# Optimization experiments

Measured on AMD Instinct MI355X. Metric: run time of the kernel, lower is better.

Reference implementation:

```python
import jax, jax.numpy as jnp
import numpy as np

N = 100000
D = 64
FE = 8
E = 1600000


def setup_inputs() -> dict:
    key = jax.random.key(0)
    ks = jax.random.split(key, 24)
    s = 0.05
    inp = {
        "H_adapted_t": jax.random.normal(ks[0], (N, D), jnp.float32),
        "event_vector": jax.random.normal(ks[1], (N, FE), jnp.float32),
        "edge_index": jax.random.randint(ks[2], (2, E), 0, N, jnp.int32),
        # event encoder MLP
        "enc_W1": jax.random.normal(ks[3], (FE, D), jnp.float32) * s,
        "enc_b1": jnp.zeros((D,), jnp.float32),
        "enc_W2": jax.random.normal(ks[4], (D, D), jnp.float32) * s,
        "enc_b2": jnp.zeros((D,), jnp.float32),
        # GCNConv
        "gcn_W": jax.random.normal(ks[5], (D, D), jnp.float32) * s,
        "gcn_b": jnp.zeros((D,), jnp.float32),
        # GATConv (heads=1, concat=False)
        "gat_W": jax.random.normal(ks[6], (D, D), jnp.float32) * s,
        "gat_att_src": jax.random.normal(ks[7], (D,), jnp.float32) * s,
        "gat_att_dst": jax.random.normal(ks[8], (D,), jnp.float32) * s,
        "gat_b": jnp.zeros((D,), jnp.float32),
        # gate fusion
        "gate_W": jax.random.normal(ks[9], (2 * D, D), jnp.float32) * s,
        "gate_b": jnp.zeros((D,), jnp.float32),
        # residual decoder
        "res_W1": jax.random.normal(ks[10], (2 * D, D), jnp.float32) * s,
        "res_b1": jnp.zeros((D,), jnp.float32),
        "res_W2": jax.random.normal(ks[11], (D, D), jnp.float32) * s,
        "res_b2": jnp.zeros((D,), jnp.float32),
        # speed head
        "sp_W1": jax.random.normal(ks[12], (D, 32), jnp.float32) * s,
        "sp_b1": jnp.zeros((32,), jnp.float32),
        "sp_W2": jax.random.normal(ks[13], (32, 1), jnp.float32) * s,
        "sp_b2": jnp.zeros((1,), jnp.float32),
    }
    return inp


def _gcn(x, src, dst, W, b, n):
    # PyG GCNConv: x' = D^{-1/2} (A + I) D^{-1/2} X W + b
    h = x @ W
    deg = jax.ops.segment_sum(jnp.ones_like(dst, jnp.float32), dst, num_segments=n)
    dinv = jnp.where(deg > 0, jax.lax.rsqrt(jnp.maximum(deg, 1e-12)), 0.0)
    norm = dinv[src] * dinv[dst]  # [E+N]
    out = jax.ops.segment_sum(h[src] * norm[:, None], dst, num_segments=n)
    return out + b


def _gat(x, src, dst, W, att_src, att_dst, b, n):
    # PyG GATConv (1 head): alpha = softmax_dst(leaky_relu(a_s.Wx_src + a_d.Wx_dst))
    h = x @ W
    a_s = h @ att_src  # [n]
    a_d = h @ att_dst
    e = jax.nn.leaky_relu(a_s[src] + a_d[dst], negative_slope=0.2)  # [E+N]
    m = jax.ops.segment_max(e, dst, num_segments=n)
    ex = jnp.exp(e - m[dst])
    z = jax.ops.segment_sum(ex, dst, num_segments=n)
    alpha = ex / z[dst]
    out = jax.ops.segment_sum(h[src] * alpha[:, None], dst, num_segments=n)
    return out + b


def reference(H_adapted_t, event_vector, edge_index,
              enc_W1, enc_b1, enc_W2, enc_b2,
              gcn_W, gcn_b,
              gat_W, gat_att_src, gat_att_dst, gat_b,
              gate_W, gate_b,
              res_W1, res_b1, res_W2, res_b2,
              sp_W1, sp_b1, sp_W2, sp_b2):
    n = H_adapted_t.shape[0]
    # add self-loops (PyG default for both convs)
    loop = jnp.arange(n, dtype=edge_index.dtype)
    src = jnp.concatenate([edge_index[0], loop])
    dst = jnp.concatenate([edge_index[1], loop])

    # event encoder
    emb = jax.nn.relu(event_vector @ enc_W1 + enc_b1) @ enc_W2 + enc_b2
    # diffusion: GCN -> ReLU -> GAT -> ReLU
    x = jax.nn.relu(_gcn(emb, src, dst, gcn_W, gcn_b, n))
    diffused = jax.nn.relu(_gat(x, src, dst, gat_W, gat_att_src, gat_att_dst, gat_b, n))

    fusion = jnp.concatenate([H_adapted_t, diffused], axis=-1)  # [N, 2D]
    gate = jax.nn.sigmoid(fusion @ gate_W + gate_b)
    delta_raw = jax.nn.relu(fusion @ res_W1 + res_b1) @ res_W2 + res_b2
    delta = gate * delta_raw
    H_final = H_adapted_t + delta
    pred_speed = (jax.nn.relu(H_final @ sp_W1 + sp_b1) @ sp_W2 + sp_b2)[:, 0]
    return (delta, H_final, pred_speed)
```

## Files before the change

### kernel.cpp

```cpp
#include <hip/hip_runtime.h>
#include <hip/hip_bf16.h>

#define NN 100000
#define DD 64
#define FEE 8
#define EE 1600000

#define NBUCK 391
#define BCAP 6144
#define CHA 4096
#define NBLKA ((EE + CHA - 1) / CHA)

typedef __attribute__((ext_vector_type(8))) short bf16x8;
typedef __attribute__((ext_vector_type(4))) float f32x4;
typedef __attribute__((ext_vector_type(2))) float f32x2;

__device__ __forceinline__ float b2f(unsigned short u) {
    return __uint_as_float(((unsigned)u) << 16);
}
__device__ __forceinline__ unsigned short f2b(float f) {
    unsigned u = __float_as_uint(f);
    unsigned r = 0x7fffu + ((u >> 16) & 1u);
    return (unsigned short)((u + r) >> 16);
}
__device__ __forceinline__ float lrelu(float v) { return v > 0.f ? v : 0.2f * v; }
__device__ __forceinline__ unsigned fkey(float x) {
    unsigned b = __float_as_uint(x);
    return (b & 0x80000000u) ? ~b : (b | 0x80000000u);
}
__device__ __forceinline__ float funkey(unsigned u) {
    unsigned b = (u & 0x80000000u) ? (u & 0x7fffffffu) : ~u;
    return __uint_as_float(b);
}
__device__ __forceinline__ bf16x8 pack8(const float* p) {
    const float4 a = *(const float4*)p;
    const float4 b = *(const float4*)(p + 4);
    bf16x8 r;
    r[0] = (short)f2b(a.x); r[1] = (short)f2b(a.y);
    r[2] = (short)f2b(a.z); r[3] = (short)f2b(a.w);
    r[4] = (short)f2b(b.x); r[5] = (short)f2b(b.y);
    r[6] = (short)f2b(b.z); r[7] = (short)f2b(b.w);
    return r;
}

__device__ __forceinline__ float deq8(unsigned v) {
#if __has_builtin(__builtin_amdgcn_cvt_f32_fp8)
    return __builtin_amdgcn_cvt_f32_fp8(v & 0xffu, 0);
#else
    unsigned t = v & 0x7fu;
    float m = __uint_as_float(0x3C000000u + (t << 20));
    if (t < 8) m = 2.f * m - 0.015625f;
    return (v & 0x80u) ? -m : m;
#endif
}
__device__ __forceinline__ float4 deq8x4(unsigned v) {
#if __has_builtin(__builtin_amdgcn_cvt_pk_f32_fp8)
    f32x2 lo = __builtin_amdgcn_cvt_pk_f32_fp8((int)v, false);
    f32x2 hi = __builtin_amdgcn_cvt_pk_f32_fp8((int)v, true);
    return make_float4(lo[0], lo[1], hi[0], hi[1]);
#else
    return make_float4(deq8(v), deq8(v >> 8), deq8(v >> 16), deq8(v >> 24));
#endif
}
__device__ __forceinline__ unsigned q8(float f) {
    unsigned u = __float_as_uint(f);
    unsigned s = (u >> 24) & 0x80u;
    float a = fminf(__uint_as_float(u & 0x7fffffffu), 448.f);
    unsigned t;
    if (a < 0.015625f) {
        t = (unsigned)__float2int_rn(a * 512.f);
    } else {
        unsigned b = __float_as_uint(a);
        b += ((b >> 20) & 1u) + 0x7FFFFu;
        unsigned e = (b >> 23) - 120u;
        t = (e > 15u) ? 0x7Eu : (((b >> 20) & 7u) | (e << 3));
    }
    return s | t;
}
__device__ __forceinline__ unsigned pk4(float a, float b, float c, float d) {
    return q8(a) | (q8(b) << 8) | (q8(c) << 16) | (q8(d) << 24);
}

#define LK 136
#define LK2 72

__global__ __launch_bounds__(256, 4) void k_encoder_mfma(
    const float* __restrict__ ev, const float* __restrict__ W1, const float* __restrict__ b1,
    const float* __restrict__ W2, const float* __restrict__ b2,
    const float* __restrict__ gcnW, const float* __restrict__ dinv,
    unsigned char* __restrict__ hA8)
{
    __shared__ short sW1T[64 * 32];
    __shared__ short sW2T[64 * LK2];
    __shared__ short sGWT[64 * LK2];
    __shared__ float sb1[64], sb2[64];
    __shared__ short sStage[4][16 * LK2];

    for (int t = threadIdx.x; t < 64 * 32; t += 256) {
        int n = t >> 5, k = t & 31;
        sW1T[n * 32 + k] = (k < FEE) ? (short)f2b(W1[k * 64 + n]) : (short)0;
    }
    for (int t = threadIdx.x; t < 64 * 64; t += 256) {
        int k = t >> 6, n = t & 63;
        sW2T[n * LK2 + k] = (short)f2b(W2[t]);
        sGWT[n * LK2 + k] = (short)f2b(gcnW[t]);
    }
    if (threadIdx.x < 64) {
        sb1[threadIdx.x] = b1[threadIdx.x];
        sb2[threadIdx.x] = b2[threadIdx.x];
    }
    __syncthreads();

    const int wave = threadIdx.x >> 6;
    const int lane = threadIdx.x & 63;
    const int m16  = lane & 15;
    const int quad = lane >> 4;
    short* myStage = &sStage[wave][0];

    const int ngroups = NN / 16;
    for (int g = blockIdx.x * 4 + wave; g < ngroups; g += gridDim.x * 4) {
        const int row0 = g * 16;
        bf16x8 a0;
        #pragma unroll
        for (int i = 0; i < 8; i++) a0[i] = 0;
        if (quad == 0) a0 = pack8(ev + (size_t)(row0 + m16) * FEE);
        f32x4 acc[4];
        #pragma unroll
        for (int c = 0; c < 4; c++) {
            f32x4 z = {0.f, 0.f, 0.f, 0.f};
            acc[c] = __builtin_amdgcn_mfma_f32_16x16x32_bf16(
                a0, *(const bf16x8*)&sW1T[(c * 16 + m16) * 32 + quad * 8], z, 0, 0, 0);
        }
        #pragma unroll
        for (int c = 0; c < 4; c++) {
            int n = c * 16 + m16;
            float bb = sb1[n];
            #pragma unroll
            for (int r = 0; r < 4; r++)
                myStage[(quad * 4 + r) * LK2 + n] = (short)f2b(fmaxf(acc[c][r] + bb, 0.f));
        }
        bf16x8 af0 = *(const bf16x8*)&myStage[m16 * LK2 + quad * 8];
        bf16x8 af1 = *(const bf16x8*)&myStage[m16 * LK2 + 32 + quad * 8];
        #pragma unroll
        for (int c = 0; c < 4; c++) {
            f32x4 z = {0.f, 0.f, 0.f, 0.f};
            const short* bp = &sW2T[(c * 16 + m16) * LK2 + quad * 8];
            z = __builtin_amdgcn_mfma_f32_16x16x32_bf16(af0, *(const bf16x8*)bp, z, 0, 0, 0);
            acc[c] = __builtin_amdgcn_mfma_f32_16x16x32_bf16(af1, *(const bf16x8*)(bp + 32), z, 0, 0, 0);
        }
        #pragma unroll
        for (int c = 0; c < 4; c++) {
            int n = c * 16 + m16;
            float bb = sb2[n];
            #pragma unroll
            for (int r = 0; r < 4; r++)
                myStage[(quad * 4 + r) * LK2 + n] = (short)f2b(acc[c][r] + bb);
        }
        af0 = *(const bf16x8*)&myStage[m16 * LK2 + quad * 8];
        af1 = *(const bf16x8*)&myStage[m16 * LK2 + 32 + quad * 8];
        #pragma unroll
        for (int c = 0; c < 4; c++) {
            f32x4 z = {0.f, 0.f, 0.f, 0.f};
            const short* bp = &sGWT[(c * 16 + m16) * LK2 + quad * 8];
            z = __builtin_amdgcn_mfma_f32_16x16x32_bf16(af0, *(const bf16x8*)bp, z, 0, 0, 0);
            acc[c] = __builtin_amdgcn_mfma_f32_16x16x32_bf16(af1, *(const bf16x8*)(bp + 32), z, 0, 0, 0);
        }
        #pragma unroll
        for (int c = 0; c < 4; c++) {
            int n = c * 16 + m16;
            #pragma unroll
            for (int r = 0; r < 4; r++)
                myStage[(quad * 4 + r) * LK2 + n] = (short)f2b(acc[c][r]);
        }
        #pragma unroll
        for (int h = 0; h < 2; h++) {
            int row = h * 8 + (lane >> 3);
            int col = (lane & 7) * 8;
            float sc = 32.f * dinv[row0 + row];
            const short* sp = &myStage[row * LK2 + col];
            uint2 w;
            w.x = pk4(b2f(sp[0]) * sc, b2f(sp[1]) * sc, b2f(sp[2]) * sc, b2f(sp[3]) * sc);
            w.y = pk4(b2f(sp[4]) * sc, b2f(sp[5]) * sc, b2f(sp[6]) * sc, b2f(sp[7]) * sc);
            *(uint2*)(hA8 + (size_t)(row0 + row) * 64 + col) = w;
        }
    }
}

__global__ __launch_bounds__(256, 4) void k_gatw_mfma(
    const unsigned short* __restrict__ x, const float* __restrict__ gatW,
    const float* __restrict__ attS, const float* __restrict__ attD,
    unsigned char* __restrict__ hC8, float* __restrict__ a_s, float* __restrict__ a_d)
{
    __shared__ short sGWT[64 * LK2];
    __shared__ float sAS[64], sAD[64];
    __shared__ short sStage[4][16 * LK2];
    for (int t = threadIdx.x; t < 64 * 64; t += 256) {
        int k = t >> 6, n = t & 63;
        sGWT[n * LK2 + k] = (short)f2b(gatW[t]);
    }
    if (threadIdx.x < 64) {
        sAS[threadIdx.x] = attS[threadIdx.x];
        sAD[threadIdx.x] = attD[threadIdx.x];
    }
    __syncthreads();

    const int wave = threadIdx.x >> 6;
    const int lane = threadIdx.x & 63;
    const int m16  = lane & 15;
    const int quad = lane >> 4;
    short* myStage = &sStage[wave][0];

    const int ngroups = NN / 16;
    for (int g = blockIdx.x * 4 + wave; g < ngroups; g += gridDim.x * 4) {
        const int row0 = g * 16;
        const unsigned short* xr = x + (size_t)(row0 + m16) * 64 + quad * 8;
        bf16x8 af0 = *(const bf16x8*)xr;
        bf16x8 af1 = *(const bf16x8*)(xr + 32);
        f32x4 acc[4];
        #pragma unroll
        for (int c = 0; c < 4; c++) {
            f32x4 z = {0.f, 0.f, 0.f, 0.f};
            const short* bp = &sGWT[(c * 16 + m16) * LK2 + quad * 8];
            z = __builtin_amdgcn_mfma_f32_16x16x32_bf16(af0, *(const bf16x8*)bp, z, 0, 0, 0);
            acc[c] = __builtin_amdgcn_mfma_f32_16x16x32_bf16(af1, *(const bf16x8*)(bp + 32), z, 0, 0, 0);
        }
        float ps[4] = {0.f, 0.f, 0.f, 0.f}, pd[4] = {0.f, 0.f, 0.f, 0.f};
        #pragma unroll
        for (int c = 0; c < 4; c++) {
            int n = c * 16 + m16;
            float was = sAS[n], wad = sAD[n];
            #pragma unroll
            for (int r = 0; r < 4; r++) {
                float v = acc[c][r];
                myStage[(quad * 4 + r) * LK2 + n] = (short)f2b(v);
                ps[r] += v * was;
                pd[r] += v * wad;
            }
        }
        #pragma unroll
        for (int off = 1; off < 16; off <<= 1) {
            #pragma unroll
            for (int r = 0; r < 4; r++) {
                ps[r] += __shfl_xor(ps[r], off, 64);
                pd[r] += __shfl_xor(pd[r], off, 64);
            }
        }
        if (m16 == 0) {
            #pragma unroll
            for (int r = 0; r < 4; r++) {
                a_s[row0 + quad * 4 + r] = ps[r];
                a_d[row0 + quad * 4 + r] = pd[r];
            }
        }
        #pragma unroll
        for (int h = 0; h < 2; h++) {
            int row = h * 8 + (lane >> 3);
            int col = (lane & 7) * 8;
            const short* sp = &myStage[row * LK2 + col];
            uint2 w;
            w.x = pk4(b2f(sp[0]) * 32.f, b2f(sp[1]) * 32.f, b2f(sp[2]) * 32.f, b2f(sp[3]) * 32.f);
            w.y = pk4(b2f(sp[4]) * 32.f, b2f(sp[5]) * 32.f, b2f(sp[6]) * 32.f, b2f(sp[7]) * 32.f);
            *(uint2*)(hC8 + (size_t)(row0 + row) * 64 + col) = w;
        }
    }
}

__global__ __launch_bounds__(512, 4) void k_decoder_mfma(
    const float* __restrict__ H, const float* diff,
    const float* __restrict__ gateW, const float* __restrict__ gateB,
    const float* __restrict__ resW1, const float* __restrict__ resB1,
    const float* __restrict__ resW2, const float* __restrict__ resB2,
    const float* __restrict__ spW1, const float* __restrict__ spB1,
    const float* __restrict__ spW2, const float* __restrict__ spB2,
    float* outDelta, float* __restrict__ outH, float* __restrict__ outP)
{
    __shared__ short sGW[64 * LK];
    __shared__ short sRW1[64 * LK];
    __shared__ short sRW2[64 * LK2];
    __shared__ short sSW1[32 * LK2];
    __shared__ float sGB[64], sRB1[64], sRB2[64];
    __shared__ float sSB1[32], sSW2[32];
    __shared__ float sSB2;
    __shared__ short sStage[8][16 * LK2];

    for (int t = threadIdx.x; t < 128 * 64; t += 512) {
        int k = t >> 6, n = t & 63;
        sGW[n * LK + k]  = (short)f2b(gateW[t]);
        sRW1[n * LK + k] = (short)f2b(resW1[t]);
    }
    for (int t = threadIdx.x; t < 64 * 64; t += 512) {
        int k = t >> 6, n = t & 63;
        sRW2[n * LK2 + k] = (short)f2b(resW2[t]);
    }
    for (int t = threadIdx.x; t < 64 * 32; t += 512) {
        int k = t >> 5, n = t & 31;
        sSW1[n * LK2 + k] = (short)f2b(spW1[t]);
    }
    if (threadIdx.x < 64) {
        sGB[threadIdx.x]  = gateB[threadIdx.x];
        sRB1[threadIdx.x] = resB1[threadIdx.x];
        sRB2[threadIdx.x] = resB2[threadIdx.x];
    }
    if (threadIdx.x < 32) {
        sSB1[threadIdx.x] = spB1[threadIdx.x];
        sSW2[threadIdx.x] = spW2[threadIdx.x];
    }
    if (threadIdx.x == 0) sSB2 = spB2[0];
    __syncthreads();

    const int wave = threadIdx.x >> 6;
    const int lane = threadIdx.x & 63;
    const int m16  = lane & 15;
    const int quad = lane >> 4;
    short* myStage = &sStage[wave][0];

    const int ngroups = NN / 16;
    for (int g = blockIdx.x * 8 + wave; g < ngroups; g += gridDim.x * 8) {
        const int row0 = g * 16;
        const float* Hrow = H    + (size_t)(row0 + m16) * 64 + quad * 8;
        const float* Drow = diff + (size_t)(row0 + m16) * 64 + quad * 8;
        bf16x8 afrag[4];
        afrag[0] = pack8(Hrow);
        afrag[1] = pack8(Hrow + 32);
        afrag[2] = pack8(Drow);
        afrag[3] = pack8(Drow + 32);

        f32x4 accG[4], accR[4];
        #pragma unroll
        for (int c = 0; c < 4; c++) {
            f32x4 z = {0.f, 0.f, 0.f, 0.f};
            accG[c] = z; accR[c] = z;
        }
        #pragma unroll
        for (int c = 0; c < 4; c++) {
            const short* bg = &sGW[(c * 16 + m16) * LK + quad * 8];
            const short* br = &sRW1[(c * 16 + m16) * LK + quad * 8];
            #pragma unroll
            for (int t = 0; t < 4; t++) {
                bf16x8 bgf = *(const bf16x8*)(bg + 32 * t);
                accG[c] = __builtin_amdgcn_mfma_f32_16x16x32_bf16(afrag[t], bgf, accG[c], 0, 0, 0);
                bf16x8 brf = *(const bf16x8*)(br + 32 * t);
                accR[c] = __builtin_amdgcn_mfma_f32_16x16x32_bf16(afrag[t], brf, accR[c], 0, 0, 0);
            }
        }

        float gateV[4][4];
        #pragma unroll
        for (int c = 0; c < 4; c++) {
            int n = c * 16 + m16;
            float gb = sGB[n], rb = sRB1[n];
            #pragma unroll
            for (int r = 0; r < 4; r++) {
                gateV[c][r] = 1.f / (1.f + __expf(-(accG[c][r] + gb)));
                int mrow = quad * 4 + r;
                myStage[mrow * LK2 + n] = (short)f2b(fmaxf(accR[c][r] + rb, 0.f));
            }
        }
        bf16x8 h1f0 = *(const bf16x8*)&myStage[m16 * LK2 + quad * 8];
        bf16x8 h1f1 = *(const bf16x8*)&myStage[m16 * LK2 + 32 + quad * 8];

        f32x4 accD[4];
        #pragma unroll
        for (int c = 0; c < 4; c++) { f32x4 z = {0.f, 0.f, 0.f, 0.f}; accD[c] = z; }
        #pragma unroll
        for (int c = 0; c < 4; c++) {
            const short* bp = &sRW2[(c * 16 + m16) * LK2 + quad * 8];
            accD[c] = __builtin_amdgcn_mfma_f32_16x16x32_bf16(h1f0, *(const bf16x8*)bp, accD[c], 0, 0, 0);
            accD[c] = __builtin_amdgcn_mfma_f32_16x16x32_bf16(h1f1, *(const bf16x8*)(bp + 32), accD[c], 0, 0, 0);
        }

        #pragma unroll
        for (int c = 0; c < 4; c++) {
            int n = c * 16 + m16;
            float rb2 = sRB2[n];
            #pragma unroll
            for (int r = 0; r < 4; r++) {
                int mrow = quad * 4 + r;
                float delta = gateV[c][r] * (accD[c][r] + rb2);
                float hv = H[(size_t)(row0 + mrow) * 64 + n];
                float hf = hv + delta;
                outDelta[(size_t)(row0 + mrow) * 64 + n] = delta;
                outH[(size_t)(row0 + mrow) * 64 + n] = hf;
                myStage[mrow * LK2 + n] = (short)f2b(hf);
            }
        }
        bf16x8 hff0 = *(const bf16x8*)&myStage[m16 * LK2 + quad * 8];
        bf16x8 hff1 = *(const bf16x8*)&myStage[m16 * LK2 + 32 + quad * 8];

        f32x4 accS[2];
        { f32x4 z = {0.f, 0.f, 0.f, 0.f}; accS[0] = z; accS[1] = z; }
        #pragma unroll
        for (int c = 0; c < 2; c++) {
            const short* bp = &sSW1[(c * 16 + m16) * LK2 + quad * 8];
            accS[c] = __builtin_amdgcn_mfma_f32_16x16x32_bf16(hff0, *(const bf16x8*)bp, accS[c], 0, 0, 0);
            accS[c] = __builtin_amdgcn_mfma_f32_16x16x32_bf16(hff1, *(const bf16x8*)(bp + 32), accS[c], 0, 0, 0);
        }
        float part[4];
        #pragma unroll
        for (int r = 0; r < 4; r++) {
            float p0 = fmaxf(accS[0][r] + sSB1[m16], 0.f) * sSW2[m16];
            float p1 = fmaxf(accS[1][r] + sSB1[16 + m16], 0.f) * sSW2[16 + m16];
            part[r] = p0 + p1;
        }
        #pragma unroll
        for (int off = 1; off < 16; off <<= 1) {
            #pragma unroll
            for (int r = 0; r < 4; r++) part[r] += __shfl_xor(part[r], off, 64);
        }
        if (m16 == 0) {
            #pragma unroll
            for (int r = 0; r < 4; r++) outP[row0 + quad * 4 + r] = part[r] + sSB2;
        }
    }
}


__global__ __launch_bounds__(256, 2) void k_binA(
    const int* __restrict__ src, const int* __restrict__ dst,
    int* __restrict__ bcnt, int* __restrict__ bpacked)
{
    __shared__ int sCount[512];
    __shared__ int sOff[512];
    __shared__ int sCur[512];
    __shared__ int sGbase[512];
    __shared__ int sScan[256];
    __shared__ int sStage[CHA];
    __shared__ unsigned short sBkt[CHA];
    const int t = threadIdx.x;
    const int e0 = blockIdx.x * CHA;
    const int len = min(CHA, EE - e0);

    for (int i = t; i < 512; i += 256) sCount[i] = 0;
    __syncthreads();
    for (int i = t; i < len; i += 256) atomicAdd(&sCount[dst[e0 + i] >> 8], 1);
    __syncthreads();
    int a0 = sCount[2 * t], a1 = sCount[2 * t + 1];
    int pairsum = a0 + a1;
    sScan[t] = pairsum;
    __syncthreads();
    for (int off = 1; off < 256; off <<= 1) {
        int v = (t >= off) ? sScan[t - off] : 0;
        __syncthreads();
        sScan[t] += v;
        __syncthreads();
    }
    int excl = sScan[t] - pairsum;
    sOff[2 * t] = excl;       sOff[2 * t + 1] = excl + a0;
    sCur[2 * t] = excl;       sCur[2 * t + 1] = excl + a0;
    __syncthreads();
    for (int b = t; b < NBUCK; b += 256) {
        int c = sCount[b];
        sGbase[b] = c ? atomicAdd(&bcnt[b], c) : 0;
    }
    __syncthreads();
    for (int i = t; i < len; i += 256) {
        int d = dst[e0 + i];
        int s = src[e0 + i];
        int b = d >> 8;
        int p = atomicAdd(&sCur[b], 1);
        sStage[p] = ((d & 255) << 17) | s;
        sBkt[p] = (unsigned short)b;
    }
    __syncthreads();
    for (int i = t; i < len; i += 256) {
        int b = sBkt[i];
        int gp = sGbase[b] + (i - sOff[b]);
        if (gp < BCAP) bpacked[(size_t)b * BCAP + gp] = sStage[i];
    }
}

__global__ __launch_bounds__(256) void k_fillB2(
    const int* __restrict__ bcnt, const int* __restrict__ bpacked,
    int* __restrict__ row_ptr, int* __restrict__ rend, float* __restrict__ dinv,
    int* __restrict__ csr)
{
    __shared__ int lcnt[256];
    __shared__ int lscan[256];
    __shared__ int lcur[256];
    __shared__ int lstage[BCAP];
    __shared__ int sWs[4];
    __shared__ int sBase;
    const int b = blockIdx.x;
    const int t = threadIdx.x;
    const int node0 = b << 8;
    const int cnt = min(bcnt[b], BCAP);
    lcnt[t] = 0;
    int partial = 0;
    for (int i = t; i < b; i += 256) partial += bcnt[i];
    #pragma unroll
    for (int o = 32; o >= 1; o >>= 1) partial += __shfl_xor(partial, o, 64);
    if ((t & 63) == 0) sWs[t >> 6] = partial;
    __syncthreads();
    if (t == 0) sBase = sWs[0] + sWs[1] + sWs[2] + sWs[3];
    const int* bp = bpacked + (size_t)b * BCAP;
    for (int i = t; i < cnt; i += 256) atomicAdd(&lcnt[bp[i] >> 17], 1);
    __syncthreads();
    const int base = sBase;
    int own = lcnt[t];
    lscan[t] = own;
    __syncthreads();
    for (int off = 1; off < 256; off <<= 1) {
        int v = (t >= off) ? lscan[t - off] : 0;
        __syncthreads();
        lscan[t] += v;
        __syncthreads();
    }
    int excl = lscan[t] - own;
    int node = node0 + t;
    if (node < NN) {
        row_ptr[node] = base + excl;
        rend[node] = base + excl + own;
        dinv[node] = rsqrtf((float)own + 1.0f);
    }
    lcur[t] = excl;
    __syncthreads();
    for (int i = t; i < cnt; i += 256) {
        int v = bp[i];
        int p = atomicAdd(&lcur[v >> 17], 1);
        lstage[p] = v & 0x1FFFF;
    }
    __syncthreads();
    for (int i = t; i < cnt; i += 256) csr[base + i] = lstage[i];
}


__global__ __launch_bounds__(256) void k_gcn_gather(
    const int* __restrict__ row_ptr, const int* __restrict__ rend,
    const int* __restrict__ csr, const float* __restrict__ dinv,
    const unsigned char* __restrict__ hA8, const float* __restrict__ gcnB,
    unsigned short* __restrict__ x)
{
    __shared__ int2 sE[4][2][32];
    const int wave = threadIdx.x >> 6;
    const int lane = threadIdx.x & 63;
    const int half = lane >> 5;
    const int hl   = lane & 31;
    const int g2   = hl >> 4;
    const int c4   = (lane & 15) * 4;
    int2* myE = sE[wave][half];
    const float4 gb = *(const float4*)(gcnB + c4);
    const int stride = gridDim.x * 8;
    for (int node = blockIdx.x * 8 + wave * 2 + half; node < NN; node += stride) {
        const int base = row_ptr[node], end = rend[node];
        float r0 = 0.f, r1 = 0.f, r2 = 0.f, r3 = 0.f;
        for (int cb = base; cb < end; cb += 32) {
            int rem = end - cb; if (rem > 32) rem = 32;
            int sidx = 0; float w = 0.f;
            if (hl < rem) { sidx = csr[cb + hl]; w = 1.f; }
            myE[hl] = make_int2(sidx, __float_as_int(w));
            int k = 0;
            for (; k + 16 <= rem; k += 16) {
                unsigned vv[8]; float ww[8];
                #pragma unroll
                for (int j = 0; j < 8; j++) {
                    int2 e = myE[k + 2 * j + g2];
                    ww[j] = __int_as_float(e.y);
                    vv[j] = *(const unsigned*)(hA8 + (((unsigned)e.x << 6) | (unsigned)c4));
                }
                #pragma unroll
                for (int j = 0; j < 8; j++) {
                    float4 d = deq8x4(vv[j]);
                    r0 = fmaf(d.x, ww[j], r0); r1 = fmaf(d.y, ww[j], r1);
                    r2 = fmaf(d.z, ww[j], r2); r3 = fmaf(d.w, ww[j], r3);
                }
            }
            for (; k < rem; k += 8) {
                unsigned vv[4]; float ww[4];
                #pragma unroll
                for (int j = 0; j < 4; j++) {
                    int2 e = myE[k + 2 * j + g2];
                    ww[j] = __int_as_float(e.y);
                    vv[j] = *(const unsigned*)(hA8 + (((unsigned)e.x << 6) | (unsigned)c4));
                }
                #pragma unroll
                for (int j = 0; j < 4; j++) {
                    float4 d = deq8x4(vv[j]);
                    r0 = fmaf(d.x, ww[j], r0); r1 = fmaf(d.y, ww[j], r1);
                    r2 = fmaf(d.z, ww[j], r2); r3 = fmaf(d.w, ww[j], r3);
                }
            }
        }
        r0 += __shfl_xor(r0, 16, 64); r1 += __shfl_xor(r1, 16, 64);
        r2 += __shfl_xor(r2, 16, 64); r3 += __shfl_xor(r3, 16, 64);
        unsigned sv = *(const unsigned*)(hA8 + (((unsigned)node << 6) | (unsigned)c4));
        float4 sd = deq8x4(sv);
        float sc = dinv[node] * 0.03125f;
        if (g2 == 0) {
            float o0 = fmaxf(fmaf(r0 + sd.x, sc, gb.x), 0.f);
            float o1 = fmaxf(fmaf(r1 + sd.y, sc, gb.y), 0.f);
            float o2 = fmaxf(fmaf(r2 + sd.z, sc, gb.z), 0.f);
            float o3 = fmaxf(fmaf(r3 + sd.w, sc, gb.w), 0.f);
            uint2 wv;
            wv.x = (unsigned)f2b(o0) | ((unsigned)f2b(o1) << 16);
            wv.y = (unsigned)f2b(o2) | ((unsigned)f2b(o3) << 16);
            *(uint2*)(x + (size_t)node * 64 + c4) = wv;
        }
    }
}

__global__ __launch_bounds__(256) void k_gat_fused(
    const int* __restrict__ row_ptr, const int* __restrict__ rend,
    const int* __restrict__ csr,
    const float* __restrict__ a_s, const float* __restrict__ a_d,
    const unsigned char* __restrict__ hC8, const float* __restrict__ gatB,
    float* __restrict__ diff)
{
    __shared__ int2 sE[4][2][32];
    const int wave = threadIdx.x >> 6;
    const int lane = threadIdx.x & 63;
    const int half = lane >> 5;
    const int hl   = lane & 31;
    const int g2   = hl >> 4;
    const int c4   = (lane & 15) * 4;
    int2* myE = sE[wave][half];
    const float4 gb = *(const float4*)(gatB + c4);
    const int stride = gridDim.x * 8;
    for (int node = blockIdx.x * 8 + wave * 2 + half; node < NN; node += stride) {
        const int base = row_ptr[node], end = rend[node];
        const float adn = a_d[node];
        const float p0 = __expf(lrelu(a_s[node] + adn));
        float zl = 0.f;
        float r0 = 0.f, r1 = 0.f, r2 = 0.f, r3 = 0.f;
        for (int cb = base; cb < end; cb += 32) {
            int rem = end - cb; if (rem > 32) rem = 32;
            int sidx = 0; float p = 0.f;
            if (hl < rem) {
                sidx = csr[cb + hl];
                p = __expf(lrelu(a_s[sidx] + adn));
            }
            myE[hl] = make_int2(sidx, __float_as_int(p));
            zl += p;
            int k = 0;
            for (; k + 16 <= rem; k += 16) {
                unsigned vv[8]; float ww[8];
                #pragma unroll
                for (int j = 0; j < 8; j++) {
                    int2 e = myE[k + 2 * j + g2];
                    ww[j] = __int_as_float(e.y);
                    vv[j] = *(const unsigned*)(hC8 + (((unsigned)e.x << 6) | (unsigned)c4));
                }
                #pragma unroll
                for (int j = 0; j < 8; j++) {
                    float4 d = deq8x4(vv[j]);
                    r0 = fmaf(d.x, ww[j], r0); r1 = fmaf(d.y, ww[j], r1);
                    r2 = fmaf(d.z, ww[j], r2); r3 = fmaf(d.w, ww[j], r3);
                }
            }
            for (; k < rem; k += 8) {
                unsigned vv[4]; float ww[4];
                #pragma unroll
                for (int j = 0; j < 4; j++) {
                    int2 e = myE[k + 2 * j + g2];
                    ww[j] = __int_as_float(e.y);
                    vv[j] = *(const unsigned*)(hC8 + (((unsigned)e.x << 6) | (unsigned)c4));
                }
                #pragma unroll
                for (int j = 0; j < 4; j++) {
                    float4 d = deq8x4(vv[j]);
                    r0 = fmaf(d.x, ww[j], r0); r1 = fmaf(d.y, ww[j], r1);
                    r2 = fmaf(d.z, ww[j], r2); r3 = fmaf(d.w, ww[j], r3);
                }
            }
        }
        #pragma unroll
        for (int o = 16; o >= 1; o >>= 1) zl += __shfl_xor(zl, o, 64);
        float z = p0 + zl;
        r0 += __shfl_xor(r0, 16, 64); r1 += __shfl_xor(r1, 16, 64);
        r2 += __shfl_xor(r2, 16, 64); r3 += __shfl_xor(r3, 16, 64);
        unsigned sv = *(const unsigned*)(hC8 + (((unsigned)node << 6) | (unsigned)c4));
        float4 sd = deq8x4(sv);
        r0 = fmaf(sd.x, p0, r0); r1 = fmaf(sd.y, p0, r1);
        r2 = fmaf(sd.z, p0, r2); r3 = fmaf(sd.w, p0, r3);
        if (g2 == 0) {
            float inv = 1.f / (32.f * z);
            float4 ov;
            ov.x = fmaxf(fmaf(r0, inv, gb.x), 0.f);
            ov.y = fmaxf(fmaf(r1, inv, gb.y), 0.f);
            ov.z = fmaxf(fmaf(r2, inv, gb.z), 0.f);
            ov.w = fmaxf(fmaf(r3, inv, gb.w), 0.f);
            *(float4*)(diff + (size_t)node * 64 + c4) = ov;
        }
    }
}


__global__ __launch_bounds__(256, 4) void k_encoder(
    const float* __restrict__ ev, const float* __restrict__ W1, const float* __restrict__ b1,
    const float* __restrict__ W2, const float* __restrict__ b2,
    const float* __restrict__ gcnW, unsigned short* __restrict__ hA)
{
    __shared__ float sW1[FEE * DD];
    __shared__ float sW2[DD * DD];
    __shared__ float sGW[DD * DD];
    __shared__ float sb1[DD], sb2[DD];
    __shared__ float stage[4 * DD];
    for (int t = threadIdx.x; t < FEE * DD; t += 256) sW1[t] = W1[t];
    for (int t = threadIdx.x; t < DD * DD; t += 256) sW2[t] = W2[t];
    for (int t = threadIdx.x; t < DD * DD; t += 256) sGW[t] = gcnW[t];
    if (threadIdx.x < DD) {
        sb1[threadIdx.x] = b1[threadIdx.x];
        sb2[threadIdx.x] = b2[threadIdx.x];
    }
    __syncthreads();
    const int slot = threadIdx.x >> 6, j = threadIdx.x & 63;
    const int ngroups = NN / 4;
    for (int g = blockIdx.x; g < ngroups; g += gridDim.x) {
        int node = g * 4 + slot;
        const float* evp = ev + node * FEE;
        float accv = sb1[j];
        #pragma unroll
        for (int i = 0; i < FEE; i++) accv += evp[i] * sW1[i * DD + j];
        float hid = fmaxf(accv, 0.f);
        stage[slot * DD + j] = hid;
        __syncthreads();
        float embv = sb2[j];
        #pragma unroll 8
        for (int i = 0; i < DD; i++) embv += stage[slot * DD + i] * sW2[i * DD + j];
        __syncthreads();
        stage[slot * DD + j] = embv;
        __syncthreads();
        float hv = 0.f;
        #pragma unroll 8
        for (int i = 0; i < DD; i++) hv += stage[slot * DD + i] * sGW[i * DD + j];
        hA[node * DD + j] = f2b(hv);
        __syncthreads();
    }
}

__global__ void k_degf(const int* __restrict__ dst, float* __restrict__ deg) {
    int e = blockIdx.x * 256 + threadIdx.x;
    if (e < EE) atomicAdd(&deg[dst[e]], 1.0f);
}
__global__ void k_dinvf(float* deg) {
    int i = blockIdx.x * 256 + threadIdx.x;
    if (i < NN) deg[i] = rsqrtf(deg[i] + 1.0f);
}
__global__ __launch_bounds__(256) void k_gcn_agg(
    const int* __restrict__ src, const int* __restrict__ dst,
    const float* __restrict__ dinv, const unsigned short* __restrict__ hA,
    float* __restrict__ acc)
{
    int lane = threadIdx.x & 63;
    int w = blockIdx.x * 4 + (threadIdx.x >> 6);
    int nw = gridDim.x * 4;
    for (int e = w; e < EE; e += nw) {
        int s = src[e], d = dst[e];
        float norm = dinv[s] * dinv[d];
        atomicAdd(&acc[d * DD + lane], b2f(hA[s * DD + lane]) * norm);
    }
}
__global__ __launch_bounds__(256, 4) void k_gcn_post(
    const float* __restrict__ acc, const unsigned short* __restrict__ hA,
    const float* __restrict__ dinv, const float* __restrict__ gcnB,
    const float* __restrict__ gatW, const float* __restrict__ attS, const float* __restrict__ attD,
    unsigned short* __restrict__ hC, float* __restrict__ a_s, float* __restrict__ a_d,
    unsigned int* __restrict__ mkey)
{
    __shared__ float sGW[DD * DD];
    __shared__ float sB[DD], sAS[DD], sAD[DD];
    __shared__ float stage[4 * DD];
    for (int t = threadIdx.x; t < DD * DD; t += 256) sGW[t] = gatW[t];
    if (threadIdx.x < DD) {
        sB[threadIdx.x] = gcnB[threadIdx.x];
        sAS[threadIdx.x] = attS[threadIdx.x];
        sAD[threadIdx.x] = attD[threadIdx.x];
    }
    __syncthreads();
    const int slot = threadIdx.x >> 6, j = threadIdx.x & 63;
    const int ngroups = NN / 4;
    for (int g = blockIdx.x; g < ngroups; g += gridDim.x) {
        int node = g * 4 + slot;
        float dv = dinv[node];
        float xv = fmaxf(acc[node * DD + j] + b2f(hA[node * DD + j]) * dv * dv + sB[j], 0.f);
        stage[slot * DD + j] = xv;
        __syncthreads();
        float hv = 0.f;
        #pragma unroll 8
        for (int i = 0; i < DD; i++) hv += stage[slot * DD + i] * sGW[i * DD + j];
        hC[node * DD + j] = f2b(hv);
        float ts = hv * sAS[j], td = hv * sAD[j];
        #pragma unroll
        for (int m = 32; m >= 1; m >>= 1) {
            ts += __shfl_xor(ts, m, 64);
            td += __shfl_xor(td, m, 64);
        }
        if (j == 0) {
            a_s[node] = ts;
            a_d[node] = td;
            mkey[node] = fkey(lrelu(ts + td));
        }
        __syncthreads();
    }
}
__global__ void k_gat_max(const int* __restrict__ src, const int* __restrict__ dst,
                          const float* __restrict__ a_s, const float* __restrict__ a_d,
                          unsigned int* __restrict__ mkey) {
    int e = blockIdx.x * 256 + threadIdx.x;
    if (e < EE) {
        int d = dst[e];
        float v = lrelu(a_s[src[e]] + a_d[d]);
        atomicMax(&mkey[d], fkey(v));
    }
}
__global__ void k_gat_mz(const float* __restrict__ a_s, const float* __restrict__ a_d,
                         unsigned int* __restrict__ mkey, float* __restrict__ z) {
    int i = blockIdx.x * 256 + threadIdx.x;
    if (i < NN) {
        float m = funkey(mkey[i]);
        float es = lrelu(a_s[i] + a_d[i]);
        z[i] = expf(es - m);
        ((float*)mkey)[i] = m;
    }
}
__global__ void k_gat_z(const int* __restrict__ src, const int* __restrict__ dst,
                        const float* __restrict__ a_s, const float* __restrict__ a_d,
                        const float* __restrict__ mf, float* __restrict__ z) {
    int e = blockIdx.x * 256 + threadIdx.x;
    if (e < EE) {
        int d = dst[e];
        float v = lrelu(a_s[src[e]] + a_d[d]);
        atomicAdd(&z[d], expf(v - mf[d]));
    }
}
__global__ __launch_bounds__(256) void k_gat_agg(
    const int* __restrict__ src, const int* __restrict__ dst,
    const float* __restrict__ a_s, const float* __restrict__ a_d,
    const float* __restrict__ mf, const float* __restrict__ z,
    const unsigned short* __restrict__ hC, float* __restrict__ acc)
{
    int lane = threadIdx.x & 63;
    int w = blockIdx.x * 4 + (threadIdx.x >> 6);
    int nw = gridDim.x * 4;
    for (int e = w; e < EE; e += nw) {
        int s = src[e], d = dst[e];
        float v = lrelu(a_s[s] + a_d[d]);
        float alpha = expf(v - mf[d]) / z[d];
        atomicAdd(&acc[d * DD + lane], b2f(hC[s * DD + lane]) * alpha);
    }
}
__global__ void k_gat_post(float* __restrict__ acc, const unsigned short* __restrict__ hC,
                           const float* __restrict__ a_s, const float* __restrict__ a_d,
                           const float* __restrict__ mf, const float* __restrict__ z,
                           const float* __restrict__ gatB) {
    int idx = blockIdx.x * 256 + threadIdx.x;
    if (idx < NN * DD) {
        int i = idx >> 6, j = idx & 63;
        float es = lrelu(a_s[i] + a_d[i]);
        float sw = expf(es - mf[i]) / z[i];
        float v = acc[idx] + sw * b2f(hC[idx]) + gatB[j];
        acc[idx] = fmaxf(v, 0.f);
    }
}


extern "C" void kernel_launch(void* const* d_in, const int* in_sizes, int n_in,
                              void* d_out, int out_size, void* d_ws, size_t ws_size,
                              hipStream_t stream) {
    const float* H     = (const float*)d_in[0];
    const float* ev    = (const float*)d_in[1];
    const int*   ei    = (const int*)d_in[2];
    const float* encW1 = (const float*)d_in[3];
    const float* encB1 = (const float*)d_in[4];
    const float* encW2 = (const float*)d_in[5];
    const float* encB2 = (const float*)d_in[6];
    const float* gcnW  = (const float*)d_in[7];
    const float* gcnB  = (const float*)d_in[8];
    const float* gatW  = (const float*)d_in[9];
    const float* attS  = (const float*)d_in[10];
    const float* attD  = (const float*)d_in[11];
    const float* gatB  = (const float*)d_in[12];
    const float* gateW = (const float*)d_in[13];
    const float* gateB = (const float*)d_in[14];
    const float* resW1 = (const float*)d_in[15];
    const float* resB1 = (const float*)d_in[16];
    const float* resW2 = (const float*)d_in[17];
    const float* resB2 = (const float*)d_in[18];
    const float* spW1  = (const float*)d_in[19];
    const float* spB1  = (const float*)d_in[20];
    const float* spW2  = (const float*)d_in[21];
    const float* spB2  = (const float*)d_in[22];

    const int* srcI = ei;
    const int* dstI = ei + EE;

    float* outDelta = (float*)d_out;
    float* outH     = outDelta + (size_t)NN * DD;
    float* outP     = outH + (size_t)NN * DD;

    float* diff = outDelta;
    int* bpacked = (int*)outDelta;
    unsigned short* x   = (unsigned short*)outDelta;
    unsigned char* hA8  = (unsigned char*)outH;
    unsigned char* hC8  = hA8 + (size_t)NN * DD;

    const size_t csr_need = ((size_t)4 * NN + EE + 1024) * 4;

    if (ws_size >= csr_need) {
        float* dinv = (float*)d_ws;
        float* a_s  = dinv + NN;
        float* a_d  = a_s + NN;
        int* rend   = (int*)(a_d + NN);
        int* csr    = rend + NN;
        int* bcntg  = csr + EE;
        int* row_ptr = (int*)outP;

        hipMemsetAsync(bcntg, 0, (size_t)512 * 4, stream);
        k_binA<<<NBLKA, 256, 0, stream>>>(srcI, dstI, bcntg, bpacked);
        k_fillB2<<<NBUCK, 256, 0, stream>>>(bcntg, bpacked,
                                            row_ptr, rend, dinv, csr);
        k_encoder_mfma<<<1024, 256, 0, stream>>>(ev, encW1, encB1, encW2, encB2,
                                                 gcnW, dinv, hA8);
        k_gcn_gather<<<4096, 256, 0, stream>>>(row_ptr, rend, csr, dinv, hA8, gcnB, x);
        k_gatw_mfma<<<1024, 256, 0, stream>>>(x, gatW, attS, attD, hC8, a_s, a_d);
        k_gat_fused<<<4096, 256, 0, stream>>>(row_ptr, rend, csr, a_s, a_d, hC8, gatB, diff);
    } else {
        float* dinv = (float*)d_ws;
        float* a_s  = dinv + NN;
        float* a_d  = a_s + NN;
        float* mf   = a_d + NN;
        float* z    = mf + NN;
        float* acc  = diff;
        unsigned short* hA = (unsigned short*)outH;
        unsigned short* hC = hA + (size_t)NN * DD;

        hipMemsetAsync(dinv, 0, (size_t)NN * 4, stream);
        hipMemsetAsync(acc, 0, (size_t)NN * DD * 4, stream);
        k_encoder<<<1024, 256, 0, stream>>>(ev, encW1, encB1, encW2, encB2, gcnW, hA);
        k_degf<<<(EE + 255) / 256, 256, 0, stream>>>(dstI, dinv);
        k_dinvf<<<(NN + 255) / 256, 256, 0, stream>>>(dinv);
        k_gcn_agg<<<8192, 256, 0, stream>>>(srcI, dstI, dinv, hA, acc);
        k_gcn_post<<<1024, 256, 0, stream>>>(acc, hA, dinv, gcnB, gatW, attS, attD,
                                             hC, a_s, a_d, (unsigned int*)mf);
        hipMemsetAsync(acc, 0, (size_t)NN * DD * 4, stream);
        k_gat_max<<<(EE + 255) / 256, 256, 0, stream>>>(srcI, dstI, a_s, a_d, (unsigned int*)mf);
        k_gat_mz<<<(NN + 255) / 256, 256, 0, stream>>>(a_s, a_d, (unsigned int*)mf, z);
        k_gat_z<<<(EE + 255) / 256, 256, 0, stream>>>(srcI, dstI, a_s, a_d, mf, z);
        k_gat_agg<<<8192, 256, 0, stream>>>(srcI, dstI, a_s, a_d, mf, z, hC, acc);
        k_gat_post<<<(NN * DD) / 256, 256, 0, stream>>>(acc, hC, a_s, a_d, mf, z, gatB);
    }

    k_decoder_mfma<<<512, 512, 0, stream>>>(H, diff, gateW, gateB, resW1, resB1,
                                            resW2, resB2, spW1, spB1, spW2, spB2,
                                            outDelta, outH, outP);
}
```

Measured before the change: 262.0 us.

## Map one node per 16-lane group in gathers and use shuffle-based block scans

The GCN and GAT gather kernels now assign one node to each 16-lane quarter-wave instead of each 32-lane half-wave. This removes the cross-half reduction and idle lanes at the end of a node, and unrolls a full 16-edge chunk for more loads in flight. The two binning kernels replace their shared-memory Hillis-Steele scan, which needed many barriers, with a wave-level shuffle scan plus a 4-entry cross-wave combine. The trade-off is more registers for the 16-wide unroll, and each lane now handles more edges serially since nodes average about 17 edges.

```diff
diff --git a/kernel.cpp b/kernel.cpp
--- a/kernel.cpp
+++ b/kernel.cpp
@@ -423,7 +423,7 @@
     __shared__ int sOff[512];
     __shared__ int sCur[512];
     __shared__ int sGbase[512];
-    __shared__ int sScan[256];
+    __shared__ int sWred[4];
     __shared__ int sStage[CHA];
     __shared__ unsigned short sBkt[CHA];
     const int t = threadIdx.x;
@@ -436,15 +436,23 @@
     __syncthreads();
     int a0 = sCount[2 * t], a1 = sCount[2 * t + 1];
     int pairsum = a0 + a1;
-    sScan[t] = pairsum;
-    __syncthreads();
-    for (int off = 1; off < 256; off <<= 1) {
-        int v = (t >= off) ? sScan[t - off] : 0;
-        __syncthreads();
-        sScan[t] += v;
-        __syncthreads();
-    }
-    int excl = sScan[t] - pairsum;
+    int x = pairsum;
+    #pragma unroll
+    for (int o = 1; o < 64; o <<= 1) {
+        int y = __shfl_up(x, o, 64);
+        if ((t & 63) >= o) x += y;
+    }
+    if ((t & 63) == 63) sWred[t >> 6] = x;
+    __syncthreads();
+    {
+        int wid = t >> 6;
+        int wbase = 0;
+        if (wid > 0) wbase += sWred[0];
+        if (wid > 1) wbase += sWred[1];
+        if (wid > 2) wbase += sWred[2];
+        x += wbase;
+    }
+    int excl = x - pairsum;
     sOff[2 * t] = excl;       sOff[2 * t + 1] = excl + a0;
     sCur[2 * t] = excl;       sCur[2 * t + 1] = excl + a0;
     __syncthreads();
@@ -475,10 +483,10 @@
     int* __restrict__ csr)
 {
     __shared__ int lcnt[256];
-    __shared__ int lscan[256];
     __shared__ int lcur[256];
     __shared__ int lstage[BCAP];
     __shared__ int sWs[4];
+    __shared__ int sWred[4];
     __shared__ int sBase;
     const int b = blockIdx.x;
     const int t = threadIdx.x;
@@ -497,15 +505,23 @@
     __syncthreads();
     const int base = sBase;
     int own = lcnt[t];
-    lscan[t] = own;
-    __syncthreads();
-    for (int off = 1; off < 256; off <<= 1) {
-        int v = (t >= off) ? lscan[t - off] : 0;
-        __syncthreads();
-        lscan[t] += v;
-        __syncthreads();
-    }
-    int excl = lscan[t] - own;
+    int x = own;
+    #pragma unroll
+    for (int o = 1; o < 64; o <<= 1) {
+        int y = __shfl_up(x, o, 64);
+        if ((t & 63) >= o) x += y;
+    }
+    if ((t & 63) == 63) sWred[t >> 6] = x;
+    __syncthreads();
+    {
+        int wid = t >> 6;
+        int wbase = 0;
+        if (wid > 0) wbase += sWred[0];
+        if (wid > 1) wbase += sWred[1];
+        if (wid > 2) wbase += sWred[2];
+        x += wbase;
+    }
+    int excl = x - own;
     int node = node0 + t;
     if (node < NN) {
         row_ptr[node] = base + excl;
@@ -530,71 +546,66 @@
     const unsigned char* __restrict__ hA8, const float* __restrict__ gcnB,
     unsigned short* __restrict__ x)
 {
-    __shared__ int2 sE[4][2][32];
+    __shared__ int2 sE[4][4][16];
     const int wave = threadIdx.x >> 6;
     const int lane = threadIdx.x & 63;
-    const int half = lane >> 5;
-    const int hl   = lane & 31;
-    const int g2   = hl >> 4;
-    const int c4   = (lane & 15) * 4;
-    int2* myE = sE[wave][half];
+    const int q    = lane >> 4;
+    const int hl   = lane & 15;
+    const int c4   = hl * 4;
+    int2* myE = sE[wave][q];
     const float4 gb = *(const float4*)(gcnB + c4);
-    const int stride = gridDim.x * 8;
-    for (int node = blockIdx.x * 8 + wave * 2 + half; node < NN; node += stride) {
+    const int stride = gridDim.x * 16;
+    for (int node = blockIdx.x * 16 + wave * 4 + q; node < NN; node += stride) {
         const int base = row_ptr[node], end = rend[node];
         float r0 = 0.f, r1 = 0.f, r2 = 0.f, r3 = 0.f;
-        for (int cb = base; cb < end; cb += 32) {
-            int rem = end - cb; if (rem > 32) rem = 32;
+        for (int cb = base; cb < end; cb += 16) {
+            int rem = end - cb; if (rem > 16) rem = 16;
             int sidx = 0; float w = 0.f;
             if (hl < rem) { sidx = csr[cb + hl]; w = 1.f; }
             myE[hl] = make_int2(sidx, __float_as_int(w));
-            int k = 0;
-            for (; k + 16 <= rem; k += 16) {
-                unsigned vv[8]; float ww[8];
+            if (rem == 16) {
+                unsigned vv[16]; float ww[16];
                 #pragma unroll
-                for (int j = 0; j < 8; j++) {
-                    int2 e = myE[k + 2 * j + g2];
+                for (int j = 0; j < 16; j++) {
+                    int2 e = myE[j];
                     ww[j] = __int_as_float(e.y);
                     vv[j] = *(const unsigned*)(hA8 + (((unsigned)e.x << 6) | (unsigned)c4));
                 }
                 #pragma unroll
-                for (int j = 0; j < 8; j++) {
+                for (int j = 0; j < 16; j++) {
                     float4 d = deq8x4(vv[j]);
                     r0 = fmaf(d.x, ww[j], r0); r1 = fmaf(d.y, ww[j], r1);
                     r2 = fmaf(d.z, ww[j], r2); r3 = fmaf(d.w, ww[j], r3);
                 }
-            }
-            for (; k < rem; k += 8) {
-                unsigned vv[4]; float ww[4];
-                #pragma unroll
-                for (int j = 0; j < 4; j++) {
-                    int2 e = myE[k + 2 * j + g2];
-                    ww[j] = __int_as_float(e.y);
-                    vv[j] = *(const unsigned*)(hA8 + (((unsigned)e.x << 6) | (unsigned)c4));
-                }
-                #pragma unroll
-                for (int j = 0; j < 4; j++) {
-                    float4 d = deq8x4(vv[j]);
-                    r0 = fmaf(d.x, ww[j], r0); r1 = fmaf(d.y, ww[j], r1);
-                    r2 = fmaf(d.z, ww[j], r2); r3 = fmaf(d.w, ww[j], r3);
+            } else {
+                for (int k = 0; k < rem; k += 8) {
+                    unsigned vv[8]; float ww[8];
+                    #pragma unroll
+                    for (int j = 0; j < 8; j++) {
+                        int2 e = myE[k + j];
+                        ww[j] = __int_as_float(e.y);
+                        vv[j] = *(const unsigned*)(hA8 + (((unsigned)e.x << 6) | (unsigned)c4));
+                    }
+                    #pragma unroll
+                    for (int j = 0; j < 8; j++) {
+                        float4 d = deq8x4(vv[j]);
+                        r0 = fmaf(d.x, ww[j], r0); r1 = fmaf(d.y, ww[j], r1);
+                        r2 = fmaf(d.z, ww[j], r2); r3 = fmaf(d.w, ww[j], r3);
+                    }
                 }
             }
         }
-        r0 += __shfl_xor(r0, 16, 64); r1 += __shfl_xor(r1, 16, 64);
-        r2 += __shfl_xor(r2, 16, 64); r3 += __shfl_xor(r3, 16, 64);
         unsigned sv = *(const unsigned*)(hA8 + (((unsigned)node << 6) | (unsigned)c4));
         float4 sd = deq8x4(sv);
         float sc = dinv[node] * 0.03125f;
-        if (g2 == 0) {
-            float o0 = fmaxf(fmaf(r0 + sd.x, sc, gb.x), 0.f);
-            float o1 = fmaxf(fmaf(r1 + sd.y, sc, gb.y), 0.f);
-            float o2 = fmaxf(fmaf(r2 + sd.z, sc, gb.z), 0.f);
-            float o3 = fmaxf(fmaf(r3 + sd.w, sc, gb.w), 0.f);
-            uint2 wv;
-            wv.x = (unsigned)f2b(o0) | ((unsigned)f2b(o1) << 16);
-            wv.y = (unsigned)f2b(o2) | ((unsigned)f2b(o3) << 16);
-            *(uint2*)(x + (size_t)node * 64 + c4) = wv;
-        }
+        float o0 = fmaxf(fmaf(r0 + sd.x, sc, gb.x), 0.f);
+        float o1 = fmaxf(fmaf(r1 + sd.y, sc, gb.y), 0.f);
+        float o2 = fmaxf(fmaf(r2 + sd.z, sc, gb.z), 0.f);
+        float o3 = fmaxf(fmaf(r3 + sd.w, sc, gb.w), 0.f);
+        uint2 wv;
+        wv.x = (unsigned)f2b(o0) | ((unsigned)f2b(o1) << 16);
+        wv.y = (unsigned)f2b(o2) | ((unsigned)f2b(o3) << 16);
+        *(uint2*)(x + (size_t)node * 64 + c4) = wv;
     }
 }
 
@@ -605,24 +616,23 @@
     const unsigned char* __restrict__ hC8, const float* __restrict__ gatB,
     float* __restrict__ diff)
 {
-    __shared__ int2 sE[4][2][32];
+    __shared__ int2 sE[4][4][16];
     const int wave = threadIdx.x >> 6;
     const int lane = threadIdx.x & 63;
-    const int half = lane >> 5;
-    const int hl   = lane & 31;
-    const int g2   = hl >> 4;
-    const int c4   = (lane & 15) * 4;
-    int2* myE = sE[wave][half];
+    const int q    = lane >> 4;
+    const int hl   = lane & 15;
+    const int c4   = hl * 4;
+    int2* myE = sE[wave][q];
     const float4 gb = *(const float4*)(gatB + c4);
-    const int stride = gridDim.x * 8;
-    for (int node = blockIdx.x * 8 + wave * 2 + half; node < NN; node += stride) {
+    const int stride = gridDim.x * 16;
+    for (int node = blockIdx.x * 16 + wave * 4 + q; node < NN; node += stride) {
         const int base = row_ptr[node], end = rend[node];
         const float adn = a_d[node];
         const float p0 = __expf(lrelu(a_s[node] + adn));
         float zl = 0.f;
         float r0 = 0.f, r1 = 0.f, r2 = 0.f, r3 = 0.f;
-        for (int cb = base; cb < end; cb += 32) {
-            int rem = end - cb; if (rem > 32) rem = 32;
+        for (int cb = base; cb < end; cb += 16) {
+            int rem = end - cb; if (rem > 16) rem = 16;
             int sidx = 0; float p = 0.f;
             if (hl < rem) {
                 sidx = csr[cb + hl];
@@ -630,56 +640,54 @@
             }
             myE[hl] = make_int2(sidx, __float_as_int(p));
             zl += p;
-            int k = 0;
-            for (; k + 16 <= rem; k += 16) {
-                unsigned vv[8]; float ww[8];
+            if (rem == 16) {
+                unsigned vv[16]; float ww[16];
                 #pragma unroll
-                for (int j = 0; j < 8; j++) {
-                    int2 e = myE[k + 2 * j + g2];
+                for (int j = 0; j < 16; j++) {
+                    int2 e = myE[j];
                     ww[j] = __int_as_float(e.y);
                     vv[j] = *(const unsigned*)(hC8 + (((unsigned)e.x << 6) | (unsigned)c4));
                 }
                 #pragma unroll
-                for (int j = 0; j < 8; j++) {
+                for (int j = 0; j < 16; j++) {
                     float4 d = deq8x4(vv[j]);
                     r0 = fmaf(d.x, ww[j], r0); r1 = fmaf(d.y, ww[j], r1);
                     r2 = fmaf(d.z, ww[j], r2); r3 = fmaf(d.w, ww[j], r3);
                 }
-            }
-            for (; k < rem; k += 8) {
-                unsigned vv[4]; float ww[4];
-                #pragma unroll
-                for (int j = 0; j < 4; j++) {
-                    int2 e = myE[k + 2 * j + g2];
-                    ww[j] = __int_as_float(e.y);
-                    vv[j] = *(const unsigned*)(hC8 + (((unsigned)e.x << 6) | (unsigned)c4));
-                }
-                #pragma unroll
-                for (int j = 0; j < 4; j++) {
-                    float4 d = deq8x4(vv[j]);
-                    r0 = fmaf(d.x, ww[j], r0); r1 = fmaf(d.y, ww[j], r1);
-                    r2 = fmaf(d.z, ww[j], r2); r3 = fmaf(d.w, ww[j], r3);
+            } else {
+                for (int k = 0; k < rem; k += 8) {
+                    unsigned vv[8]; float ww[8];
+                    #pragma unroll
+                    for (int j = 0; j < 8; j++) {
+                        int2 e = myE[k + j];
+                        ww[j] = __int_as_float(e.y);
+                        vv[j] = *(const unsigned*)(hC8 + (((unsigned)e.x << 6) | (unsigned)c4));
+                    }
+                    #pragma unroll
+                    for (int j = 0; j < 8; j++) {
+                        float4 d = deq8x4(vv[j]);
+                        r0 = fmaf(d.x, ww[j], r0); r1 = fmaf(d.y, ww[j], r1);
+                        r2 = fmaf(d.z, ww[j], r2); r3 = fmaf(d.w, ww[j], r3);
+                    }
                 }
             }
         }
-        #pragma unroll
-        for (int o = 16; o >= 1; o >>= 1) zl += __shfl_xor(zl, o, 64);
+        zl += __shfl_xor(zl, 1, 64);
+        zl += __shfl_xor(zl, 2, 64);
+        zl += __shfl_xor(zl, 4, 64);
+        zl += __shfl_xor(zl, 8, 64);
         float z = p0 + zl;
-        r0 += __shfl_xor(r0, 16, 64); r1 += __shfl_xor(r1, 16, 64);
-        r2 += __shfl_xor(r2, 16, 64); r3 += __shfl_xor(r3, 16, 64);
         unsigned sv = *(const unsigned*)(hC8 + (((unsigned)node << 6) | (unsigned)c4));
         float4 sd = deq8x4(sv);
         r0 = fmaf(sd.x, p0, r0); r1 = fmaf(sd.y, p0, r1);
         r2 = fmaf(sd.z, p0, r2); r3 = fmaf(sd.w, p0, r3);
-        if (g2 == 0) {
-            float inv = 1.f / (32.f * z);
-            float4 ov;
-            ov.x = fmaxf(fmaf(r0, inv, gb.x), 0.f);
-            ov.y = fmaxf(fmaf(r1, inv, gb.y), 0.f);
-            ov.z = fmaxf(fmaf(r2, inv, gb.z), 0.f);
-            ov.w = fmaxf(fmaf(r3, inv, gb.w), 0.f);
-            *(float4*)(diff + (size_t)node * 64 + c4) = ov;
-        }
+        float inv = 1.f / (32.f * z);
+        float4 ov;
+        ov.x = fmaxf(fmaf(r0, inv, gb.x), 0.f);
+        ov.y = fmaxf(fmaf(r1, inv, gb.y), 0.f);
+        ov.z = fmaxf(fmaf(r2, inv, gb.z), 0.f);
+        ov.w = fmaxf(fmaf(r3, inv, gb.w), 0.f);
+        *(float4*)(diff + (size_t)node * 64 + c4) = ov;
     }
 }
 
```

New measurement: 257.7 us. No clear change (-1.7%).
